# Performance work log

Hardware: AMD Instinct MI355X
Metric: run time of the kernel (lower is better)

## Reference

```python
import jax, jax.numpy as jnp
import numpy as np

B, S, D = 2, 2048, 1024
H, DK, DV = 16, 64, 64
EPS = 1e-5
SQRT_DK = float(np.sqrt(DK))


def setup_inputs() -> dict:
    key = jax.random.key(0)
    ks = jax.random.split(key, 8)
    sc = 0.02
    return {
        "x": jax.random.normal(ks[0], (B, S, D), jnp.float32),
        "Wk": jax.random.normal(ks[1], (D, H * DK), jnp.float32) * sc,
        "bk": jnp.zeros((H * DK,), jnp.float32),
        "Wq": jax.random.normal(ks[2], (D, H * DK), jnp.float32) * sc,
        "bq": jnp.zeros((H * DK,), jnp.float32),
        "Wv": jax.random.normal(ks[3], (D, H * DV), jnp.float32) * sc,
        "bv": jnp.zeros((H * DV,), jnp.float32),
        "Wo": jax.random.normal(ks[4], (H * DV, D), jnp.float32) * sc,
        "bo": jnp.zeros((D,), jnp.float32),
        "gamma": jnp.ones((D,), jnp.float32),
        "beta": jnp.zeros((D,), jnp.float32),
    }


def reference(x, Wk, bk, Wq, bq, Wv, bv, Wo, bo, gamma, beta):
    b, s, d = x.shape
    # NOTE: original torch code reshapes (B, S, H*dk) directly to (B, H, S, dk)
    # without a transpose; we replicate that exact (non-standard) reshape.
    keys = (x @ Wk + bk).reshape(b, H, s, DK)
    queries = (x @ Wq + bq).reshape(b, H, s, DK)
    values = (x @ Wv + bv).reshape(b, H, s, DV)

    scores = jnp.einsum('bhqd,bhkd->bhqk', queries, keys) / SQRT_DK
    causal_mask = jnp.triu(jnp.ones((s, s), bool), k=1)  # True = masked
    scores = jnp.where(causal_mask[None, None], jnp.float32(-1e9), scores)
    attention = jax.nn.softmax(scores, axis=-1)

    context = jnp.einsum('bhqk,bhkd->bhqd', attention, values)
    context = context.reshape(b, s, H * DV)

    out = context @ Wo + bo  # dropout is identity at inference
    out = out + x            # residual connection

    mean = jnp.mean(out, axis=-1, keepdims=True)
    var = jnp.mean(jnp.square(out - mean), axis=-1, keepdims=True)
    return (out - mean) / jnp.sqrt(var + EPS) * gamma + beta
```

## Files before the change

kernel.cpp:

```cpp
#include <hip/hip_runtime.h>


typedef __attribute__((ext_vector_type(8))) __bf16 bf16x8;
typedef __attribute__((ext_vector_type(8))) unsigned short ushort8;
typedef __attribute__((ext_vector_type(4))) unsigned short u16x4;
typedef __attribute__((ext_vector_type(4))) float f32x4;
typedef __attribute__((ext_vector_type(4))) unsigned int u32x4;

static __device__ __forceinline__ unsigned short f2bf(float f) {
    unsigned u = __builtin_bit_cast(unsigned, f);
    u += 0x7fffu + ((u >> 16) & 1u);
    return (unsigned short)(u >> 16);
}

static __device__ __forceinline__ float bf2f(unsigned short u) {
    return __builtin_bit_cast(float, (unsigned)u << 16);
}

static __device__ __forceinline__ unsigned cvt_pk_bf16(float lo, float hi) {
    unsigned r;
    asm("v_cvt_pk_bf16_f32 %0, %1, %2" : "=v"(r) : "v"(lo), "v"(hi));
    return r;
}

__global__ __launch_bounds__(256) void prep_kernel(
    const float* __restrict__ x,
    const float* __restrict__ Wq, const float* __restrict__ Wk,
    const float* __restrict__ Wv, const float* __restrict__ Wo,
    unsigned short* __restrict__ xb, unsigned short* __restrict__ WT)
{
    const int tid = threadIdx.x;
    const int z = blockIdx.z;
    if (z == 4) {
        const int bid = blockIdx.y * 16 + blockIdx.x;
        const int base = bid * 4096 + tid;
        #pragma unroll
        for (int it = 0; it < 16; it++) {
            int i = base + it * 256;
            float4 v = ((const float4*)x)[i];
            ushort4 o;
            o.x = f2bf(v.x); o.y = f2bf(v.y); o.z = f2bf(v.z); o.w = f2bf(v.w);
            ((ushort4*)xb)[i] = o;
        }
        return;
    }
    const float* src = (z == 0) ? Wq : (z == 1) ? Wk : (z == 2) ? Wv : Wo;
    unsigned short* dst = WT + ((size_t)z << 20);
    __shared__ __align__(16) unsigned short t[64 * 68];
    const int n0 = blockIdx.x * 64, k0 = blockIdx.y * 64;
    #pragma unroll
    for (int u = 0; u < 4; u++) {
        int e = u * 256 + tid;
        int r = e >> 4, c4 = (e & 15) * 4;
        float4 v = *(const float4*)(src + (k0 + r) * 1024 + n0 + c4);
        ushort4 o;
        o.x = f2bf(v.x); o.y = f2bf(v.y); o.z = f2bf(v.z); o.w = f2bf(v.w);
        *(ushort4*)(t + r * 68 + c4) = o;
    }
    __syncthreads();
    #pragma unroll
    for (int u = 0; u < 4; u++) {
        int e = u * 256 + tid;
        int rn = e >> 4, ck = (e & 15) * 4;
        ushort4 o;
        o.x = t[(ck + 0) * 68 + rn];
        o.y = t[(ck + 1) * 68 + rn];
        o.z = t[(ck + 2) * 68 + rn];
        o.w = t[(ck + 3) * 68 + rn];
        *(ushort4*)(dst + (n0 + rn) * 1024 + k0 + ck) = o;
    }
}

__global__ __launch_bounds__(256) void vtrans_kernel(const unsigned short* __restrict__ V,
                                                     unsigned short* __restrict__ VT) {
    __shared__ __align__(16) unsigned short t[64 * 68];
    const int tid = threadIdx.x;
    const int p0 = blockIdx.x * 64;
    const long base = (long)blockIdx.y * 131072;
    #pragma unroll
    for (int u = 0; u < 2; u++) {
        int e = u * 256 + tid;
        int r = e >> 3, c8 = (e & 7) * 8;
        ushort8 v = *(const ushort8*)(V + base + (long)(p0 + r) * 64 + c8);
        *(ushort8*)(t + r * 68 + c8) = v;
    }
    __syncthreads();
    #pragma unroll
    for (int u = 0; u < 4; u++) {
        int e = u * 256 + tid;
        int dv = e >> 4, pk = (e & 15) * 4;
        ushort4 o;
        o.x = t[(pk + 0) * 68 + dv];
        o.y = t[(pk + 1) * 68 + dv];
        o.z = t[(pk + 2) * 68 + dv];
        o.w = t[(pk + 3) * 68 + dv];
        *(ushort4*)(VT + base + (long)dv * 2048 + p0 + pk) = o;
    }
}

__global__ __launch_bounds__(256, 3) void gemm_kernel(
    const unsigned short* __restrict__ A,
    const unsigned short* __restrict__ Bt,
    const float* __restrict__ b0, const float* __restrict__ b1, const float* __restrict__ b2,
    unsigned short* __restrict__ outQ, unsigned short* __restrict__ outK,
    unsigned short* __restrict__ outV,
    const float* __restrict__ resid, int mode)
{
    __shared__ __align__(16) unsigned short As[2][128 * 32];
    __shared__ __align__(16) unsigned short Bs[2][128 * 32];
    const int tid = threadIdx.x;
    const int lane = tid & 63, wave = tid >> 6;
    const int quad = lane >> 4, l16 = lane & 15;
    const int wm = wave >> 1, wn = wave & 1;
    const int row0 = blockIdx.y * 128, n0g = blockIdx.x * 128;

    const int sr = tid >> 2;
    const int sc = (tid & 3) * 8;
    const unsigned short* Ag0 = A + (size_t)(row0 + sr) * 1024 + sc;
    const unsigned short* Ag1 = A + (size_t)(row0 + 64 + sr) * 1024 + sc;
    const unsigned short* Bg0 = Bt + (size_t)(n0g + sr) * 1024 + sc;
    const unsigned short* Bg1 = Bt + (size_t)(n0g + 64 + sr) * 1024 + sc;

    {
        ushort8 a0 = *(const ushort8*)(Ag0);
        ushort8 a1 = *(const ushort8*)(Ag1);
        ushort8 bv0 = *(const ushort8*)(Bg0);
        ushort8 bv1 = *(const ushort8*)(Bg1);
        *(ushort8*)(As[0] + sr * 32 + sc) = a0;
        *(ushort8*)(As[0] + (64 + sr) * 32 + sc) = a1;
        *(ushort8*)(Bs[0] + sr * 32 + sc) = bv0;
        *(ushort8*)(Bs[0] + (64 + sr) * 32 + sc) = bv1;
    }
    __syncthreads();

    f32x4 acc[4][4] = {};
    #pragma unroll 2
    for (int it = 0; it < 32; ++it) {
        const int cur = it & 1;
        ushort8 na0, na1, nb0, nb1;
        if (it < 31) {
            const int k0 = (it + 1) * 32;
            na0 = *(const ushort8*)(Ag0 + k0);
            na1 = *(const ushort8*)(Ag1 + k0);
            nb0 = *(const ushort8*)(Bg0 + k0);
            nb1 = *(const ushort8*)(Bg1 + k0);
        }
        bf16x8 af[4], bfr[4];
        #pragma unroll
        for (int i = 0; i < 4; i++)
            af[i] = *(const bf16x8*)(As[cur] + (wm * 64 + i * 16 + l16) * 32 + quad * 8);
        #pragma unroll
        for (int j = 0; j < 4; j++)
            bfr[j] = *(const bf16x8*)(Bs[cur] + (wn * 64 + j * 16 + l16) * 32 + quad * 8);
        #pragma unroll
        for (int i = 0; i < 4; i++)
            #pragma unroll
            for (int j = 0; j < 4; j++)
                acc[i][j] = __builtin_amdgcn_mfma_f32_16x16x32_bf16(af[i], bfr[j], acc[i][j], 0, 0, 0);
        if (it < 31) {
            const int nxt = cur ^ 1;
            *(ushort8*)(As[nxt] + sr * 32 + sc) = na0;
            *(ushort8*)(As[nxt] + (64 + sr) * 32 + sc) = na1;
            *(ushort8*)(Bs[nxt] + sr * 32 + sc) = nb0;
            *(ushort8*)(Bs[nxt] + (64 + sr) * 32 + sc) = nb1;
            __syncthreads();
        }
    }

    if (mode == 0) {
        const int which = n0g >> 10;
        const float* bp = (which == 0) ? b0 : (which == 1) ? b1 : b2;
        unsigned short* op = (which == 0) ? outQ : (which == 1) ? outK : outV;
        const float scl = (which == 0) ? 0.125f : 1.0f;
        #pragma unroll
        for (int i = 0; i < 4; i++)
            #pragma unroll
            for (int j = 0; j < 4; j++) {
                int c = (n0g + wn * 64 + j * 16 + l16) & 1023;
                float bj = bp[c];
                #pragma unroll
                for (int r = 0; r < 4; r++) {
                    int r_g = row0 + wm * 64 + i * 16 + quad * 4 + r;
                    op[(size_t)r_g * 1024 + c] = f2bf((acc[i][j][r] + bj) * scl);
                }
            }
    } else {
        #pragma unroll
        for (int i = 0; i < 4; i++)
            #pragma unroll
            for (int j = 0; j < 4; j++) {
                int c_g = n0g + wn * 64 + j * 16 + l16;
                float bj = b0[c_g];
                #pragma unroll
                for (int r = 0; r < 4; r++) {
                    int r_g = row0 + wm * 64 + i * 16 + quad * 4 + r;
                    size_t idx = (size_t)r_g * 1024 + c_g;
                    outQ[idx] = f2bf(acc[i][j][r] + bj + resid[idx]);
                }
            }
    }
}

__global__ __launch_bounds__(256, 4) void flash_kernel(
    const unsigned short* __restrict__ Q,
    const unsigned short* __restrict__ K,
    const unsigned short* __restrict__ VT,
    unsigned short* __restrict__ Ctx)
{
    __shared__ __align__(16) unsigned short Kt[128 * 72];
    __shared__ __align__(16) unsigned short Vt[64 * 136];
    const int tid = threadIdx.x;
    const int lane = tid & 63, wave = tid >> 6;
    const int quad = lane >> 4, l16 = lane & 15;
    const int y = blockIdx.y;
    const int qb = (y < 8) ? (31 - y) : (y < 16) ? (y - 8)
                 : (y < 24) ? (39 - y) : (y - 16);
    const int q0 = qb * 64;
    const long base = (long)blockIdx.x * 131072;
    const int nt = (qb + 2) >> 1;

    bf16x8 qa[2];
    #pragma unroll
    for (int h = 0; h < 2; h++)
        qa[h] = *(const bf16x8*)(Q + base + (q0 + wave * 16 + l16) * 64 + h * 32 + quad * 8);

    f32x4 o[4] = {};
    float l_one = 0.f;
    const int qpos = q0 + wave * 16 + l16;

    #pragma unroll
    for (int u = 0; u < 4; u++) {
        int e = u * 256 + tid;
        int r = e >> 3, c = (e & 7) * 8;
        *(ushort8*)(Kt + r * 72 + c) = *(const ushort8*)(K + base + (long)r * 64 + c);
        int dv = e >> 4, kc = (e & 15) * 8;
        *(ushort8*)(Vt + dv * 136 + kc) = *(const ushort8*)(VT + base + (long)dv * 2048 + kc);
    }
    __syncthreads();

    for (int t = 0; t < nt; t++) {
        ushort8 nk[4], nv[4];
        if (t + 1 < nt) {
            const int k1 = (t + 1) * 128;
            #pragma unroll
            for (int u = 0; u < 4; u++) {
                int e = u * 256 + tid;
                int r = e >> 3, c = (e & 7) * 8;
                nk[u] = *(const ushort8*)(K + base + (long)(k1 + r) * 64 + c);
                int dv = e >> 4, kc = (e & 15) * 8;
                nv[u] = *(const ushort8*)(VT + base + (long)dv * 2048 + k1 + kc);
            }
        }
        const int k0 = t * 128;
        const bool diag = (t == nt - 1);
        const int kkmax = diag ? ((q0 - k0 + wave * 16 + 15) >> 5) : 3;

        #pragma unroll
        for (int kk = 0; kk < 4; kk++) {
            if (kk <= kkmax) {
                const int cE = kk * 2, cO = kk * 2 + 1;
                f32x4 aE = {}, aO = {};
                {
                    bf16x8 kb0 = *(const bf16x8*)(Kt + (cE * 16 + l16) * 72 + quad * 8);
                    bf16x8 kb1 = *(const bf16x8*)(Kt + (cE * 16 + l16) * 72 + 32 + quad * 8);
                    aE = __builtin_amdgcn_mfma_f32_16x16x32_bf16(kb0, qa[0], aE, 0, 0, 0);
                    aE = __builtin_amdgcn_mfma_f32_16x16x32_bf16(kb1, qa[1], aE, 0, 0, 0);
                }
                {
                    bf16x8 kb0 = *(const bf16x8*)(Kt + (cO * 16 + l16) * 72 + quad * 8);
                    bf16x8 kb1 = *(const bf16x8*)(Kt + (cO * 16 + l16) * 72 + 32 + quad * 8);
                    aO = __builtin_amdgcn_mfma_f32_16x16x32_bf16(kb0, qa[0], aO, 0, 0, 0);
                    aO = __builtin_amdgcn_mfma_f32_16x16x32_bf16(kb1, qa[1], aO, 0, 0, 0);
                }
                float pE[4], pO[4];
                #pragma unroll
                for (int r = 0; r < 4; r++) {
                    float e1 = __expf(aE[r]);
                    float e2 = __expf(aO[r]);
                    if (diag) {
                        int kE = k0 + cE * 16 + quad * 4 + r;
                        int kO = k0 + cO * 16 + quad * 4 + r;
                        e1 = (kE > qpos) ? 0.f : e1;
                        e2 = (kO > qpos) ? 0.f : e2;
                    }
                    pE[r] = e1; pO[r] = e2;
                }
                l_one += (pE[0] + pE[1]) + (pE[2] + pE[3])
                       + (pO[0] + pO[1]) + (pO[2] + pO[3]);
                unsigned w0 = cvt_pk_bf16(pE[0], pE[1]);
                unsigned w1 = cvt_pk_bf16(pE[2], pE[3]);
                unsigned w2 = cvt_pk_bf16(pO[0], pO[1]);
                unsigned w3 = cvt_pk_bf16(pO[2], pO[3]);
                asm("v_permlane32_swap_b32 %0, %1" : "+v"(w0), "+v"(w2));
                asm("v_permlane16_swap_b32 %0, %1" : "+v"(w0), "+v"(w2));
                asm("v_permlane32_swap_b32 %0, %1" : "+v"(w1), "+v"(w3));
                asm("v_permlane16_swap_b32 %0, %1" : "+v"(w1), "+v"(w3));
                u32x4 pu;
                pu[0] = w0; pu[1] = w1; pu[2] = w2; pu[3] = w3;
                bf16x8 pa = __builtin_bit_cast(bf16x8, pu);
                #pragma unroll
                for (int c2 = 0; c2 < 4; c2++) {
                    bf16x8 vb = *(const bf16x8*)(Vt + (c2 * 16 + l16) * 136 + kk * 32 + quad * 8);
                    o[c2] = __builtin_amdgcn_mfma_f32_16x16x32_bf16(pa, vb, o[c2], 0, 0, 0);
                }
            }
        }
        __syncthreads();
        if (t + 1 < nt) {
            #pragma unroll
            for (int u = 0; u < 4; u++) {
                int e = u * 256 + tid;
                int r = e >> 3, c = (e & 7) * 8;
                *(ushort8*)(Kt + r * 72 + c) = nk[u];
                int dv = e >> 4, kc = (e & 15) * 8;
                *(ushort8*)(Vt + dv * 136 + kc) = nv[u];
            }
            __syncthreads();
        }
    }

    l_one += __shfl_xor(l_one, 16, 64);
    l_one += __shfl_xor(l_one, 32, 64);
    float rinv[4];
    #pragma unroll
    for (int r = 0; r < 4; r++)
        rinv[r] = 1.0f / __shfl(l_one, quad * 4 + r, 16);
    #pragma unroll
    for (int c2 = 0; c2 < 4; c2++)
        #pragma unroll
        for (int r = 0; r < 4; r++) {
            int row = q0 + wave * 16 + quad * 4 + r;
            Ctx[base + (long)row * 64 + c2 * 16 + l16] = f2bf(o[c2][r] * rinv[r]);
        }
}

__global__ __launch_bounds__(256) void ln_kernel(const unsigned short* __restrict__ inp,
                                                 const float* __restrict__ gamma,
                                                 const float* __restrict__ beta,
                                                 float* __restrict__ out)
{
    __shared__ float ssum[4], ssq[4];
    const int row = blockIdx.x;
    const int tid = threadIdx.x;
    ushort4 uv = ((const ushort4*)(inp + (size_t)row * 1024))[tid];
    float vx = bf2f(uv.x), vy = bf2f(uv.y), vz = bf2f(uv.z), vw = bf2f(uv.w);
    float s = vx + vy + vz + vw;
    float q = vx * vx + vy * vy + vz * vz + vw * vw;
    #pragma unroll
    for (int off = 32; off >= 1; off >>= 1) {
        s += __shfl_xor(s, off, 64);
        q += __shfl_xor(q, off, 64);
    }
    if ((tid & 63) == 0) { ssum[tid >> 6] = s; ssq[tid >> 6] = q; }
    __syncthreads();
    float ts = ssum[0] + ssum[1] + ssum[2] + ssum[3];
    float tq = ssq[0] + ssq[1] + ssq[2] + ssq[3];
    float mean = ts * (1.f / 1024.f);
    float var = tq * (1.f / 1024.f) - mean * mean;
    float rinv = rsqrtf(var + 1e-5f);
    float4 g = ((const float4*)gamma)[tid];
    float4 b = ((const float4*)beta)[tid];
    float4 o;
    o.x = (vx - mean) * rinv * g.x + b.x;
    o.y = (vy - mean) * rinv * g.y + b.y;
    o.z = (vz - mean) * rinv * g.z + b.z;
    o.w = (vw - mean) * rinv * g.w + b.w;
    ((float4*)(out + (size_t)row * 1024))[tid] = o;
}

extern "C" void kernel_launch(void* const* d_in, const int* in_sizes, int n_in,
                              void* d_out, int out_size, void* d_ws, size_t ws_size,
                              hipStream_t stream) {
    const float* x     = (const float*)d_in[0];
    const float* Wk    = (const float*)d_in[1];
    const float* bk    = (const float*)d_in[2];
    const float* Wq    = (const float*)d_in[3];
    const float* bq    = (const float*)d_in[4];
    const float* Wv    = (const float*)d_in[5];
    const float* bv    = (const float*)d_in[6];
    const float* Wo    = (const float*)d_in[7];
    const float* bo    = (const float*)d_in[8];
    const float* gamma = (const float*)d_in[9];
    const float* beta  = (const float*)d_in[10];
    float* out = (float*)d_out;

    char* ws = (char*)d_ws;
    unsigned short* xb    = (unsigned short*)(ws);
    unsigned short* WqkvT = (unsigned short*)(ws + (8ull << 20));
    unsigned short* Qb    = (unsigned short*)(ws + (16ull << 20));
    unsigned short* Kb    = (unsigned short*)(ws + (24ull << 20));
    unsigned short* VbT   = (unsigned short*)(ws + (32ull << 20));
    unsigned short* Cb    = (unsigned short*)(ws + (40ull << 20));
    unsigned short* outp  = (unsigned short*)(ws + (48ull << 20));
    unsigned short* WoT   = WqkvT + (3u << 20);
    unsigned short* Vbn   = Cb;

    dim3 pgrid(16, 16, 5);
    prep_kernel<<<pgrid, 256, 0, stream>>>(x, Wq, Wk, Wv, Wo, xb, WqkvT);

    dim3 qkvgrid(24, 32);
    gemm_kernel<<<qkvgrid, 256, 0, stream>>>(xb, WqkvT, bq, bk, bv,
                                             Qb, Kb, Vbn, nullptr, 0);

    dim3 vgrid(32, 32);
    vtrans_kernel<<<vgrid, 256, 0, stream>>>(Vbn, VbT);

    dim3 fgrid(32, 32);
    flash_kernel<<<fgrid, 256, 0, stream>>>(Qb, Kb, VbT, Cb);

    dim3 ogrid(8, 32);
    gemm_kernel<<<ogrid, 256, 0, stream>>>(Cb, WoT, bo, nullptr, nullptr,
                                           outp, nullptr, nullptr, x, 1);

    ln_kernel<<<4096, 256, 0, stream>>>(outp, gamma, beta, out);
}
```

Measured before the change: 197.2 us.

## Drop V transpose kernel; read V with transposing LDS loads in flash kernel

Removes the separate vtrans kernel and lets the flash kernel load V in natural row-major layout into a swizzled LDS tile. It then uses ds_read_b64_tr_b16 to produce the transposed MFMA B operand, which also lets the P operand skip the permlane swaps. This saves one kernel launch plus a full global read/write pass over V. In exchange it adds an explicit lgkmcnt wait and sched barrier in the inner loop, and relies on the XOR swizzle and lane mapping being correct.

```diff
diff --git a/kernel.cpp b/kernel.cpp
--- a/kernel.cpp
+++ b/kernel.cpp
@@ -68,33 +68,6 @@
         o.z = t[(ck + 2) * 68 + rn];
         o.w = t[(ck + 3) * 68 + rn];
         *(ushort4*)(dst + (n0 + rn) * 1024 + k0 + ck) = o;
-    }
-}
-
-__global__ __launch_bounds__(256) void vtrans_kernel(const unsigned short* __restrict__ V,
-                                                     unsigned short* __restrict__ VT) {
-    __shared__ __align__(16) unsigned short t[64 * 68];
-    const int tid = threadIdx.x;
-    const int p0 = blockIdx.x * 64;
-    const long base = (long)blockIdx.y * 131072;
-    #pragma unroll
-    for (int u = 0; u < 2; u++) {
-        int e = u * 256 + tid;
-        int r = e >> 3, c8 = (e & 7) * 8;
-        ushort8 v = *(const ushort8*)(V + base + (long)(p0 + r) * 64 + c8);
-        *(ushort8*)(t + r * 68 + c8) = v;
-    }
-    __syncthreads();
-    #pragma unroll
-    for (int u = 0; u < 4; u++) {
-        int e = u * 256 + tid;
-        int dv = e >> 4, pk = (e & 15) * 4;
-        ushort4 o;
-        o.x = t[(pk + 0) * 68 + dv];
-        o.y = t[(pk + 1) * 68 + dv];
-        o.z = t[(pk + 2) * 68 + dv];
-        o.w = t[(pk + 3) * 68 + dv];
-        *(ushort4*)(VT + base + (long)dv * 2048 + p0 + pk) = o;
     }
 }
 
@@ -204,11 +177,11 @@
 __global__ __launch_bounds__(256, 4) void flash_kernel(
     const unsigned short* __restrict__ Q,
     const unsigned short* __restrict__ K,
-    const unsigned short* __restrict__ VT,
+    const unsigned short* __restrict__ Vn,
     unsigned short* __restrict__ Ctx)
 {
     __shared__ __align__(16) unsigned short Kt[128 * 72];
-    __shared__ __align__(16) unsigned short Vt[64 * 136];
+    __shared__ __align__(16) unsigned short Vl[128 * 64];
     const int tid = threadIdx.x;
     const int lane = tid & 63, wave = tid >> 6;
     const int quad = lane >> 4, l16 = lane & 15;
@@ -228,13 +201,24 @@
     float l_one = 0.f;
     const int qpos = q0 + wave * 16 + l16;
 
+    const int vk = tid >> 3;
+    const int vws = ((tid & 7) * 16) ^ (((tid >> 3) & 3) << 5);
+    const int vwn = (tid & 7) * 8;
+    const unsigned vbase = (unsigned)(size_t)(const void*)Vl;
+    const unsigned Ab = vbase + (unsigned)((4 * quad + (l16 >> 2)) * 128 + (l16 & 3) * 8);
+    unsigned AbC[4];
+    #pragma unroll
+    for (int c2 = 0; c2 < 4; c2++)
+        AbC[c2] = Ab + ((unsigned)(c2 * 32) ^ (unsigned)((l16 >> 2) << 5));
+
     #pragma unroll
     for (int u = 0; u < 4; u++) {
         int e = u * 256 + tid;
         int r = e >> 3, c = (e & 7) * 8;
         *(ushort8*)(Kt + r * 72 + c) = *(const ushort8*)(K + base + (long)r * 64 + c);
-        int dv = e >> 4, kc = (e & 15) * 8;
-        *(ushort8*)(Vt + dv * 136 + kc) = *(const ushort8*)(VT + base + (long)dv * 2048 + kc);
+        int kr = u * 32 + vk;
+        *(ushort8*)((char*)Vl + kr * 128 + vws) =
+            *(const ushort8*)(Vn + base + (long)kr * 64 + vwn);
     }
     __syncthreads();
 
@@ -247,8 +231,7 @@
                 int e = u * 256 + tid;
                 int r = e >> 3, c = (e & 7) * 8;
                 nk[u] = *(const ushort8*)(K + base + (long)(k1 + r) * 64 + c);
-                int dv = e >> 4, kc = (e & 15) * 8;
-                nv[u] = *(const ushort8*)(VT + base + (long)dv * 2048 + k1 + kc);
+                nv[u] = *(const ushort8*)(Vn + base + (long)(k1 + u * 32 + vk) * 64 + vwn);
             }
         }
         const int k0 = t * 128;
@@ -271,6 +254,15 @@
                     bf16x8 kb1 = *(const bf16x8*)(Kt + (cO * 16 + l16) * 72 + 32 + quad * 8);
                     aO = __builtin_amdgcn_mfma_f32_16x16x32_bf16(kb0, qa[0], aO, 0, 0, 0);
                     aO = __builtin_amdgcn_mfma_f32_16x16x32_bf16(kb1, qa[1], aO, 0, 0, 0);
+                }
+                u16x4 tv[4][2];
+                #pragma unroll
+                for (int c2 = 0; c2 < 4; c2++) {
+                    unsigned a = AbC[c2] + (unsigned)(kk * 4096);
+                    asm volatile("ds_read_b64_tr_b16 %0, %1"
+                                 : "=v"(tv[c2][0]) : "v"(a));
+                    asm volatile("ds_read_b64_tr_b16 %0, %1 offset:2048"
+                                 : "=v"(tv[c2][1]) : "v"(a));
                 }
                 float pE[4], pO[4];
                 #pragma unroll
@@ -287,20 +279,22 @@
                 }
                 l_one += (pE[0] + pE[1]) + (pE[2] + pE[3])
                        + (pO[0] + pO[1]) + (pO[2] + pO[3]);
-                unsigned w0 = cvt_pk_bf16(pE[0], pE[1]);
-                unsigned w1 = cvt_pk_bf16(pE[2], pE[3]);
-                unsigned w2 = cvt_pk_bf16(pO[0], pO[1]);
-                unsigned w3 = cvt_pk_bf16(pO[2], pO[3]);
-                asm("v_permlane32_swap_b32 %0, %1" : "+v"(w0), "+v"(w2));
-                asm("v_permlane16_swap_b32 %0, %1" : "+v"(w0), "+v"(w2));
-                asm("v_permlane32_swap_b32 %0, %1" : "+v"(w1), "+v"(w3));
-                asm("v_permlane16_swap_b32 %0, %1" : "+v"(w1), "+v"(w3));
                 u32x4 pu;
-                pu[0] = w0; pu[1] = w1; pu[2] = w2; pu[3] = w3;
+                pu[0] = cvt_pk_bf16(pE[0], pE[1]);
+                pu[1] = cvt_pk_bf16(pE[2], pE[3]);
+                pu[2] = cvt_pk_bf16(pO[0], pO[1]);
+                pu[3] = cvt_pk_bf16(pO[2], pO[3]);
                 bf16x8 pa = __builtin_bit_cast(bf16x8, pu);
+                asm volatile("s_waitcnt lgkmcnt(0)" ::: "memory");
+                __builtin_amdgcn_sched_barrier(0);
                 #pragma unroll
                 for (int c2 = 0; c2 < 4; c2++) {
-                    bf16x8 vb = *(const bf16x8*)(Vt + (c2 * 16 + l16) * 136 + kk * 32 + quad * 8);
+                    ushort8 vv;
+                    vv[0] = tv[c2][0][0]; vv[1] = tv[c2][0][1];
+                    vv[2] = tv[c2][0][2]; vv[3] = tv[c2][0][3];
+                    vv[4] = tv[c2][1][0]; vv[5] = tv[c2][1][1];
+                    vv[6] = tv[c2][1][2]; vv[7] = tv[c2][1][3];
+                    bf16x8 vb = __builtin_bit_cast(bf16x8, vv);
                     o[c2] = __builtin_amdgcn_mfma_f32_16x16x32_bf16(pa, vb, o[c2], 0, 0, 0);
                 }
             }
@@ -312,8 +306,8 @@
                 int e = u * 256 + tid;
                 int r = e >> 3, c = (e & 7) * 8;
                 *(ushort8*)(Kt + r * 72 + c) = nk[u];
-                int dv = e >> 4, kc = (e & 15) * 8;
-                *(ushort8*)(Vt + dv * 136 + kc) = nv[u];
+                int kr = u * 32 + vk;
+                *(ushort8*)((char*)Vl + kr * 128 + vws) = nv[u];
             }
             __syncthreads();
         }
@@ -389,11 +383,10 @@
     unsigned short* WqkvT = (unsigned short*)(ws + (8ull << 20));
     unsigned short* Qb    = (unsigned short*)(ws + (16ull << 20));
     unsigned short* Kb    = (unsigned short*)(ws + (24ull << 20));
-    unsigned short* VbT   = (unsigned short*)(ws + (32ull << 20));
+    unsigned short* Vbn   = (unsigned short*)(ws + (32ull << 20));
     unsigned short* Cb    = (unsigned short*)(ws + (40ull << 20));
     unsigned short* outp  = (unsigned short*)(ws + (48ull << 20));
     unsigned short* WoT   = WqkvT + (3u << 20);
-    unsigned short* Vbn   = Cb;
 
     dim3 pgrid(16, 16, 5);
     prep_kernel<<<pgrid, 256, 0, stream>>>(x, Wq, Wk, Wv, Wo, xb, WqkvT);
@@ -402,11 +395,8 @@
     gemm_kernel<<<qkvgrid, 256, 0, stream>>>(xb, WqkvT, bq, bk, bv,
                                              Qb, Kb, Vbn, nullptr, 0);
 
-    dim3 vgrid(32, 32);
-    vtrans_kernel<<<vgrid, 256, 0, stream>>>(Vbn, VbT);
-
     dim3 fgrid(32, 32);
-    flash_kernel<<<fgrid, 256, 0, stream>>>(Qb, Kb, VbT, Cb);
+    flash_kernel<<<fgrid, 256, 0, stream>>>(Qb, Kb, Vbn, Cb);
 
     dim3 ogrid(8, 32);
     gemm_kernel<<<ogrid, 256, 0, stream>>>(Cb, WoT, bo, nullptr, nullptr,
```

After: 238.7 us. 21.1% more time.

## Load GEMM tiles directly into LDS with global_load_lds, single-buffered

Applied to the files above, without the earlier changes.

Replaces the register-staged, double-buffered global-to-LDS tile copy in the GEMM kernel with direct global_load_lds DMA into a single LDS buffer. The aim is to cut VGPR use and LDS-store instructions and halve LDS footprint, which could raise occupancy. In exchange the prefetch overlap is lost: each iteration now syncs, issues loads, and waits for them before computing, so global-load latency is exposed.

```diff
diff --git a/kernel.cpp b/kernel.cpp
--- a/kernel.cpp
+++ b/kernel.cpp
@@ -21,6 +21,12 @@
     unsigned r;
     asm("v_cvt_pk_bf16_f32 %0, %1, %2" : "=v"(r) : "v"(lo), "v"(hi));
     return r;
+}
+
+static __device__ __forceinline__ void gload16(const unsigned short* g, unsigned short* l) {
+    __builtin_amdgcn_global_load_lds(
+        (const __attribute__((address_space(1))) void*)g,
+        (__attribute__((address_space(3))) void*)l, 16, 0, 0);
 }
 
 __global__ __launch_bounds__(256) void prep_kernel(
@@ -106,63 +112,50 @@
     unsigned short* __restrict__ outV,
     const float* __restrict__ resid, int mode)
 {
-    __shared__ __align__(16) unsigned short As[2][128 * 32];
-    __shared__ __align__(16) unsigned short Bs[2][128 * 32];
+    __shared__ __align__(16) unsigned short As[128 * 32];
+    __shared__ __align__(16) unsigned short Bs[128 * 32];
     const int tid = threadIdx.x;
     const int lane = tid & 63, wave = tid >> 6;
     const int quad = lane >> 4, l16 = lane & 15;
     const int wm = wave >> 1, wn = wave & 1;
     const int row0 = blockIdx.y * 128, n0g = blockIdx.x * 128;
 
-    const int sr = tid >> 2;
-    const int sc = (tid & 3) * 8;
-    const unsigned short* Ag0 = A + (size_t)(row0 + sr) * 1024 + sc;
-    const unsigned short* Ag1 = A + (size_t)(row0 + 64 + sr) * 1024 + sc;
-    const unsigned short* Bg0 = Bt + (size_t)(n0g + sr) * 1024 + sc;
-    const unsigned short* Bg1 = Bt + (size_t)(n0g + 64 + sr) * 1024 + sc;
-
-    {
-        ushort8 a0 = *(const ushort8*)(Ag0);
-        ushort8 a1 = *(const ushort8*)(Ag1);
-        ushort8 bv0 = *(const ushort8*)(Bg0);
-        ushort8 bv1 = *(const ushort8*)(Bg1);
-        *(ushort8*)(As[0] + sr * 32 + sc) = a0;
-        *(ushort8*)(As[0] + (64 + sr) * 32 + sc) = a1;
-        *(ushort8*)(Bs[0] + sr * 32 + sc) = bv0;
-        *(ushort8*)(Bs[0] + (64 + sr) * 32 + sc) = bv1;
-    }
+    const int srow = wave * 32 + (lane >> 2);
+    const int scol = (lane & 3) * 8;
+    const unsigned short* Ag0 = A + (size_t)(row0 + srow) * 1024 + scol;
+    const unsigned short* Ag1 = Ag0 + (size_t)16 * 1024;
+    const unsigned short* Bg0 = Bt + (size_t)(n0g + srow) * 1024 + scol;
+    const unsigned short* Bg1 = Bg0 + (size_t)16 * 1024;
+    unsigned short* AsW = As + wave * 1024;
+    unsigned short* BsW = Bs + wave * 1024;
+
+    gload16(Ag0, AsW);
+    gload16(Ag1, AsW + 512);
+    gload16(Bg0, BsW);
+    gload16(Bg1, BsW + 512);
     __syncthreads();
 
     f32x4 acc[4][4] = {};
-    #pragma unroll 2
     for (int it = 0; it < 32; ++it) {
-        const int cur = it & 1;
-        ushort8 na0, na1, nb0, nb1;
-        if (it < 31) {
-            const int k0 = (it + 1) * 32;
-            na0 = *(const ushort8*)(Ag0 + k0);
-            na1 = *(const ushort8*)(Ag1 + k0);
-            nb0 = *(const ushort8*)(Bg0 + k0);
-            nb1 = *(const ushort8*)(Bg1 + k0);
-        }
         bf16x8 af[4], bfr[4];
         #pragma unroll
         for (int i = 0; i < 4; i++)
-            af[i] = *(const bf16x8*)(As[cur] + (wm * 64 + i * 16 + l16) * 32 + quad * 8);
+            af[i] = *(const bf16x8*)(As + (wm * 64 + i * 16 + l16) * 32 + quad * 8);
         #pragma unroll
         for (int j = 0; j < 4; j++)
-            bfr[j] = *(const bf16x8*)(Bs[cur] + (wn * 64 + j * 16 + l16) * 32 + quad * 8);
+            bfr[j] = *(const bf16x8*)(Bs + (wn * 64 + j * 16 + l16) * 32 + quad * 8);
         #pragma unroll
         for (int i = 0; i < 4; i++)
             #pragma unroll
             for (int j = 0; j < 4; j++)
                 acc[i][j] = __builtin_amdgcn_mfma_f32_16x16x32_bf16(af[i], bfr[j], acc[i][j], 0, 0, 0);
         if (it < 31) {
-            const int nxt = cur ^ 1;
-            *(ushort8*)(As[nxt] + sr * 32 + sc) = na0;
-            *(ushort8*)(As[nxt] + (64 + sr) * 32 + sc) = na1;
-            *(ushort8*)(Bs[nxt] + sr * 32 + sc) = nb0;
-            *(ushort8*)(Bs[nxt] + (64 + sr) * 32 + sc) = nb1;
+            __syncthreads();
+            const int k0 = (it + 1) * 32;
+            gload16(Ag0 + k0, AsW);
+            gload16(Ag1 + k0, AsW + 512);
+            gload16(Bg0 + k0, BsW);
+            gload16(Bg1 + k0, BsW + 512);
             __syncthreads();
         }
     }
```

After: 203.1 us. 1.03x slower.
